# Performance work log

Hardware: AMD Instinct MI355X
Metric: run time of the kernel (lower is better)

Reference implementation:

```python
import jax, jax.numpy as jnp
import numpy as np


def setup_inputs() -> dict:
    key = jax.random.key(0)
    k1, k2 = jax.random.split(key)
    B, C, N = 8, 3, 4096
    X = jax.random.normal(k1, (B, C, N), dtype=jnp.float32)
    Y = jax.random.normal(k2, (B, C, N), dtype=jnp.float32)
    return {"X": X, "Y": Y, "ps": N}


def reference(X, Y, ps):
    # X, Y: [B, C, N] -> permute to [B, N, C] point clouds
    A = jnp.transpose(X, (0, 2, 1))  # [B, N, C]
    Bp = jnp.transpose(Y, (0, 2, 1))  # [B, ps, C]
    r = jnp.sum(A * A, axis=2)[:, :, None]      # [B, N, 1]
    r1 = jnp.sum(Bp * Bp, axis=2)[:, None, :]   # [B, 1, ps]
    # squared pairwise distances: ||a||^2 - 2 a.b + ||b||^2 -> [B, N, ps]
    t = r - 2.0 * jnp.einsum('bnc,bmc->bnm', A, Bp) + r1
    d1 = jnp.min(t, axis=1)  # min over A points: [B, ps]
    d2 = jnp.min(t, axis=2)  # min over B points: [B, N]
    ls = (d1 + d2) / 2.0     # requires N == ps (as in original repeat logic)
    return jnp.mean(ls)
```

## Files before the change

### kernel.cpp

```cpp
#include <hip/hip_runtime.h>


typedef __attribute__((ext_vector_type(8))) short short8;
typedef __attribute__((ext_vector_type(16))) float f32x16;
typedef __attribute__((ext_vector_type(4))) unsigned uint4v;

constexpr int NPTS  = 4096;
constexpr int NB    = 8;
constexpr int NQ    = 2 * NB * NPTS;
constexpr int TSN   = 4;
constexpr int TGT   = 1024;
constexpr int TILES = TGT / 32;
constexpr int TPB   = 512;
constexpr int GRID_MAIN  = 16 * 4 * TSN;
constexpr int RED_BLOCKS = 64;

__device__ inline unsigned short f2bf(float x) {
    unsigned u = __float_as_uint(x);
    unsigned r = u + 0x7fff + ((u >> 16) & 1);
    return (unsigned short)(r >> 16);
}
__device__ inline float bf2f(unsigned short h) {
    return __uint_as_float(((unsigned)h) << 16);
}
__device__ inline unsigned pack2(unsigned short a, unsigned short b) {
    return (unsigned)a | ((unsigned)b << 16);
}

__global__ __launch_bounds__(TPB, 2) void chamfer_main(
    const float* __restrict__ X, const float* __restrict__ Y,
    float* __restrict__ minq)
{
    __shared__ char BL[TGT * 32];

    const int bid  = blockIdx.x;
    const int ts   = bid & 3;
    const int qg   = (bid >> 2) & 3;
    const int pair = bid >> 4;
    const int dir  = pair >> 3, b = pair & 7;
    const int tid  = threadIdx.x;
    const int lane = tid & 63, wv = tid >> 6;
    const int c    = lane & 31, h = lane >> 5;

    const float* __restrict__ Qraw = (dir ? Y : X) + b * 3 * NPTS;
    const float* __restrict__ Traw = (dir ? X : Y) + b * 3 * NPTS;

    #pragma unroll
    for (int k = 0; k < 2; ++k) {
        const int p = k * TPB + tid;
        const int i = ts * TGT + p;
        float tx = Traw[i], ty = Traw[NPTS + i], tz = Traw[2 * NPTS + i];
        float r  = fmaf(tx, tx, fmaf(ty, ty, tz * tz));
        unsigned short hx = f2bf(tx), lx = f2bf(tx - bf2f(hx));
        unsigned short hy = f2bf(ty), ly = f2bf(ty - bf2f(hy));
        unsigned short hz = f2bf(tz), lz = f2bf(tz - bf2f(hz));
        unsigned short hr = f2bf(r),  lr = f2bf(r  - bf2f(hr));
        unsigned w0 = pack2(hx, lx), w2 = pack2(hy, ly), w4 = pack2(hz, lz);
        unsigned w6 = pack2(hr, lr);
        uint4v lo = {w0, w0, w2, w2};
        uint4v hi = {w4, w4, w6, 0u};
        const int sw = (p >> 2) & 1;
        *(uint4v*)(BL + p * 32 + ((0 ^ sw) << 4)) = lo;
        *(uint4v*)(BL + p * 32 + ((1 ^ sw) << 4)) = hi;
    }

    union Frag { uint4v u; short8 s; };
    Frag qfr[4];
    float ra[4];
    #pragma unroll
    for (int s = 0; s < 4; ++s) {
        const int q = qg * 1024 + wv * 128 + s * 32 + c;
        float qx = Qraw[q], qy = Qraw[NPTS + q], qz = Qraw[2 * NPTS + q];
        ra[s] = fmaf(qx, qx, fmaf(qy, qy, qz * qz));
        float mx = -2.f * qx, my = -2.f * qy, mz = -2.f * qz;
        unsigned short hx = f2bf(mx), lx = f2bf(mx - bf2f(hx));
        unsigned short hy = f2bf(my), ly = f2bf(my - bf2f(hy));
        unsigned short hz = f2bf(mz), lz = f2bf(mz - bf2f(hz));
        uint4v f0 = {pack2(hx, hx), pack2(lx, lx), pack2(hy, hy), pack2(ly, ly)};
        uint4v f1 = {pack2(hz, hz), pack2(lz, lz), 0x3F803F80u, 0u};
        Frag f; f.u = h ? f1 : f0;
        qfr[s] = f;
    }

    __syncthreads();

    f32x16 run[4];
    #pragma unroll
    for (int s = 0; s < 4; ++s)
        #pragma unroll
        for (int i = 0; i < 16; ++i) run[s][i] = 3.4e38f;
    f32x16 zacc;
    #pragma unroll
    for (int i = 0; i < 16; ++i) zacc[i] = 0.f;

    const char* base = BL + c * 32 + ((h ^ ((c >> 2) & 1)) << 4);

    short8 tf0 = *(const short8*)(base);
    short8 tf1 = *(const short8*)(base + 1024);
    for (int t = 0; t < TILES; t += 2) {
        const int t2 = (t + 2) & (TILES - 1);
        const int t3 = (t + 3) & (TILES - 1);
        short8 nf0 = *(const short8*)(base + t2 * 1024);
        short8 nf1 = *(const short8*)(base + t3 * 1024);
        #pragma unroll
        for (int s = 0; s < 4; ++s) {
            f32x16 dA = __builtin_amdgcn_mfma_f32_32x32x16_bf16(tf0, qfr[s].s, zacc, 0, 0, 0);
            f32x16 dB = __builtin_amdgcn_mfma_f32_32x32x16_bf16(tf1, qfr[s].s, zacc, 0, 0, 0);
            #pragma unroll
            for (int i = 0; i < 16; ++i)
                run[s][i] = fminf(run[s][i], fminf(dA[i], dB[i]));
        }
        tf0 = nf0; tf1 = nf1;
    }

    #pragma unroll
    for (int s = 0; s < 4; ++s) {
        float m0 = fminf(fminf(run[s][0],  run[s][1]),  fminf(run[s][2],  run[s][3]));
        float m1 = fminf(fminf(run[s][4],  run[s][5]),  fminf(run[s][6],  run[s][7]));
        float m2 = fminf(fminf(run[s][8],  run[s][9]),  fminf(run[s][10], run[s][11]));
        float m3 = fminf(fminf(run[s][12], run[s][13]), fminf(run[s][14], run[s][15]));
        float m  = fminf(fminf(m0, m1), fminf(m2, m3));
        m = fminf(m, __shfl_xor(m, 32));
        m += ra[s];
        if (h == 0)
            minq[(size_t)ts * NQ + pair * 4096 + qg * 1024 + wv * 128 + s * 32 + c] = m;
    }
}

__global__ __launch_bounds__(256) void chamfer_reduce(
    const float4* __restrict__ mq4, float* __restrict__ partials,
    unsigned* __restrict__ counter, float* __restrict__ out)
{
    __shared__ float wsum[4];
    __shared__ int   fireFlag;
    const int tid = threadIdx.x;
    const int lane = tid & 63, wv = tid >> 6;
    const int idx = blockIdx.x * 256 + tid;

    float4 m = mq4[idx];
    #pragma unroll
    for (int s = 1; s < TSN; ++s) {
        float4 v = mq4[(size_t)s * (NQ / 4) + idx];
        m.x = fminf(m.x, v.x); m.y = fminf(m.y, v.y);
        m.z = fminf(m.z, v.z); m.w = fminf(m.w, v.w);
    }
    float v = (m.x + m.y) + (m.z + m.w);
    #pragma unroll
    for (int off = 1; off < 64; off <<= 1) v += __shfl_xor(v, off);
    if (lane == 0) wsum[wv] = v;
    __syncthreads();
    if (tid == 0) {
        partials[blockIdx.x] = (wsum[0] + wsum[1]) + (wsum[2] + wsum[3]);
        __threadfence();
        unsigned old = atomicAdd(counter, 1u);
        fireFlag = ((old & 63u) == 63u);
    }
    __syncthreads();

    if (fireFlag) {
        __threadfence();
        if (tid < 64) {
            float p = partials[tid];
            #pragma unroll
            for (int off = 1; off < 64; off <<= 1) p += __shfl_xor(p, off);
            if (tid == 0)
                out[0] = p * (1.0f / 65536.0f);
        }
    }
}

extern "C" void kernel_launch(void* const* d_in, const int* in_sizes, int n_in,
                              void* d_out, int out_size, void* d_ws, size_t ws_size,
                              hipStream_t stream) {
    const float* X = (const float*)d_in[0];
    const float* Y = (const float*)d_in[1];

    float*    minq     = (float*)d_ws;
    float*    partials = minq + (size_t)TSN * NQ;
    unsigned* counter  = (unsigned*)(partials + RED_BLOCKS);
    float*    out      = (float*)d_out;

    chamfer_main<<<GRID_MAIN, TPB, 0, stream>>>(X, Y, minq);
    chamfer_reduce<<<RED_BLOCKS, 256, 0, stream>>>(
        (const float4*)minq, partials, counter, out);
}
```

Baseline: 19.73 us.

## Fuse final reduction into main kernel via last-block atomic counter

Removes the separate reduce kernel launch. Each main block fences and increments a counter, and the last of the 256 blocks reads all partial minima, combines the four target slices and computes the mean. It also splits the running-min accumulators into two independent chains so the min after each MFMA pair has less dependency. The cost is a serial tail in which one block reduces 65536×4 floats by itself, plus higher register pressure from the doubled accumulators.

```diff
diff --git a/kernel.cpp b/kernel.cpp
--- a/kernel.cpp
+++ b/kernel.cpp
@@ -13,7 +13,6 @@
 constexpr int TILES = TGT / 32;
 constexpr int TPB   = 512;
 constexpr int GRID_MAIN  = 16 * 4 * TSN;
-constexpr int RED_BLOCKS = 64;
 
 __device__ inline unsigned short f2bf(float x) {
     unsigned u = __float_as_uint(x);
@@ -27,11 +26,14 @@
     return (unsigned)a | ((unsigned)b << 16);
 }
 
-__global__ __launch_bounds__(TPB, 2) void chamfer_main(
+__global__ __launch_bounds__(TPB, 2) void chamfer_fused(
     const float* __restrict__ X, const float* __restrict__ Y,
-    float* __restrict__ minq)
+    float* __restrict__ minq, unsigned* __restrict__ counter,
+    float* __restrict__ out)
 {
-    __shared__ char BL[TGT * 32];
+    __shared__ char  BL[TGT * 32];
+    __shared__ float wsum[8];
+    __shared__ int   fireFlag;
 
     const int bid  = blockIdx.x;
     const int ts   = bid & 3;
@@ -84,11 +86,11 @@
 
     __syncthreads();
 
-    f32x16 run[4];
+    f32x16 runA[4], runB[4];
     #pragma unroll
     for (int s = 0; s < 4; ++s)
         #pragma unroll
-        for (int i = 0; i < 16; ++i) run[s][i] = 3.4e38f;
+        for (int i = 0; i < 16; ++i) { runA[s][i] = 3.4e38f; runB[s][i] = 3.4e38f; }
     f32x16 zacc;
     #pragma unroll
     for (int i = 0; i < 16; ++i) zacc[i] = 0.f;
@@ -107,64 +109,67 @@
             f32x16 dA = __builtin_amdgcn_mfma_f32_32x32x16_bf16(tf0, qfr[s].s, zacc, 0, 0, 0);
             f32x16 dB = __builtin_amdgcn_mfma_f32_32x32x16_bf16(tf1, qfr[s].s, zacc, 0, 0, 0);
             #pragma unroll
-            for (int i = 0; i < 16; ++i)
-                run[s][i] = fminf(run[s][i], fminf(dA[i], dB[i]));
+            for (int i = 0; i < 16; ++i) {
+                runA[s][i] = fminf(runA[s][i], dA[i]);
+                runB[s][i] = fminf(runB[s][i], dB[i]);
+            }
         }
         tf0 = nf0; tf1 = nf1;
     }
 
     #pragma unroll
     for (int s = 0; s < 4; ++s) {
-        float m0 = fminf(fminf(run[s][0],  run[s][1]),  fminf(run[s][2],  run[s][3]));
-        float m1 = fminf(fminf(run[s][4],  run[s][5]),  fminf(run[s][6],  run[s][7]));
-        float m2 = fminf(fminf(run[s][8],  run[s][9]),  fminf(run[s][10], run[s][11]));
-        float m3 = fminf(fminf(run[s][12], run[s][13]), fminf(run[s][14], run[s][15]));
+        float v0 = fminf(runA[s][0],  runB[s][0]),  v1 = fminf(runA[s][1],  runB[s][1]);
+        float v2 = fminf(runA[s][2],  runB[s][2]),  v3 = fminf(runA[s][3],  runB[s][3]);
+        float v4 = fminf(runA[s][4],  runB[s][4]),  v5 = fminf(runA[s][5],  runB[s][5]);
+        float v6 = fminf(runA[s][6],  runB[s][6]),  v7 = fminf(runA[s][7],  runB[s][7]);
+        float v8 = fminf(runA[s][8],  runB[s][8]),  v9 = fminf(runA[s][9],  runB[s][9]);
+        float va = fminf(runA[s][10], runB[s][10]), vb = fminf(runA[s][11], runB[s][11]);
+        float vc = fminf(runA[s][12], runB[s][12]), vd = fminf(runA[s][13], runB[s][13]);
+        float ve = fminf(runA[s][14], runB[s][14]), vf = fminf(runA[s][15], runB[s][15]);
+        float m0 = fminf(fminf(v0, v1), fminf(v2, v3));
+        float m1 = fminf(fminf(v4, v5), fminf(v6, v7));
+        float m2 = fminf(fminf(v8, v9), fminf(va, vb));
+        float m3 = fminf(fminf(vc, vd), fminf(ve, vf));
         float m  = fminf(fminf(m0, m1), fminf(m2, m3));
         m = fminf(m, __shfl_xor(m, 32));
         m += ra[s];
         if (h == 0)
             minq[(size_t)ts * NQ + pair * 4096 + qg * 1024 + wv * 128 + s * 32 + c] = m;
     }
-}
 
-__global__ __launch_bounds__(256) void chamfer_reduce(
-    const float4* __restrict__ mq4, float* __restrict__ partials,
-    unsigned* __restrict__ counter, float* __restrict__ out)
-{
-    __shared__ float wsum[4];
-    __shared__ int   fireFlag;
-    const int tid = threadIdx.x;
-    const int lane = tid & 63, wv = tid >> 6;
-    const int idx = blockIdx.x * 256 + tid;
-
-    float4 m = mq4[idx];
-    #pragma unroll
-    for (int s = 1; s < TSN; ++s) {
-        float4 v = mq4[(size_t)s * (NQ / 4) + idx];
-        m.x = fminf(m.x, v.x); m.y = fminf(m.y, v.y);
-        m.z = fminf(m.z, v.z); m.w = fminf(m.w, v.w);
-    }
-    float v = (m.x + m.y) + (m.z + m.w);
-    #pragma unroll
-    for (int off = 1; off < 64; off <<= 1) v += __shfl_xor(v, off);
-    if (lane == 0) wsum[wv] = v;
+    __threadfence();
     __syncthreads();
     if (tid == 0) {
-        partials[blockIdx.x] = (wsum[0] + wsum[1]) + (wsum[2] + wsum[3]);
-        __threadfence();
         unsigned old = atomicAdd(counter, 1u);
-        fireFlag = ((old & 63u) == 63u);
+        fireFlag = ((old & 255u) == 255u);
     }
     __syncthreads();
 
     if (fireFlag) {
         __threadfence();
-        if (tid < 64) {
-            float p = partials[tid];
+        const float4* mq4 = (const float4*)minq;
+        float acc = 0.0f;
+        #pragma unroll
+        for (int k = 0; k < NQ / 4 / TPB; ++k) {
+            const int idx = k * TPB + tid;
+            float4 m = mq4[idx];
             #pragma unroll
-            for (int off = 1; off < 64; off <<= 1) p += __shfl_xor(p, off);
-            if (tid == 0)
-                out[0] = p * (1.0f / 65536.0f);
+            for (int s = 1; s < TSN; ++s) {
+                float4 v = mq4[s * (NQ / 4) + idx];
+                m.x = fminf(m.x, v.x); m.y = fminf(m.y, v.y);
+                m.z = fminf(m.z, v.z); m.w = fminf(m.w, v.w);
+            }
+            acc += (m.x + m.y) + (m.z + m.w);
+        }
+        #pragma unroll
+        for (int off = 1; off < 64; off <<= 1) acc += __shfl_xor(acc, off);
+        if (lane == 0) wsum[wv] = acc;
+        __syncthreads();
+        if (tid == 0) {
+            float tsum = ((wsum[0] + wsum[1]) + (wsum[2] + wsum[3]))
+                       + ((wsum[4] + wsum[5]) + (wsum[6] + wsum[7]));
+            out[0] = tsum * (1.0f / 65536.0f);
         }
     }
 }
@@ -175,12 +180,9 @@
     const float* X = (const float*)d_in[0];
     const float* Y = (const float*)d_in[1];
 
-    float*    minq     = (float*)d_ws;
-    float*    partials = minq + (size_t)TSN * NQ;
-    unsigned* counter  = (unsigned*)(partials + RED_BLOCKS);
-    float*    out      = (float*)d_out;
+    float*    minq    = (float*)d_ws;
+    unsigned* counter = (unsigned*)(minq + (size_t)TSN * NQ);
+    float*    out     = (float*)d_out;
 
-    chamfer_main<<<GRID_MAIN, TPB, 0, stream>>>(X, Y, minq);
-    chamfer_reduce<<<RED_BLOCKS, 256, 0, stream>>>(
-        (const float4*)minq, partials, counter, out);
+    chamfer_fused<<<GRID_MAIN, TPB, 0, stream>>>(X, Y, minq, counter, out);
 }
```

New measurement: 67.17 us. +240.4%, slower.
